# Performance work log

Hardware: AMD Instinct MI355X
Metric: run time of the kernel (lower is better)

## Reference

```python
import jax, jax.numpy as jnp
import numpy as np

R = 16            # DFL bins (reg_max)
C = 80            # num classes
STRIDES = (8, 16, 32)
CONF = 0.25
IOU_T = 0.45
MAX_DET = 300
K_PRE = 1024      # fixed pre-NMS candidate count (static-shape stand-in for torch's boolean mask)
CLS_OFFSET = 4096.0  # > max image coord; class-aware NMS offset (torchvision batched_nms trick)


def setup_inputs() -> dict:
    key = jax.random.key(0)
    k0, k1, k2 = jax.random.split(key, 3)
    B, CH = 16, 4 * R + C
    return {
        "p0": jax.random.normal(k0, (B, CH, 80, 80), jnp.float32),
        "p1": jax.random.normal(k1, (B, CH, 40, 40), jnp.float32),
        "p2": jax.random.normal(k2, (B, CH, 20, 20), jnp.float32),
        "h_img": 640,
        "w_img": 640,
    }


def _decode_level(p, stride):
    # p: (B, 4R+C, H, W)
    B, _, H, W = p.shape
    box_logits = p[:, : 4 * R].reshape(B, 4, R, H * W)
    bins = jnp.arange(R, dtype=p.dtype)
    # DFLIntegral: softmax over bins, expectation -> l,t,r,b distances (in stride units)
    ltrb = jnp.einsum('bkrm,r->bkm', jax.nn.softmax(box_logits, axis=2), bins) * stride  # (B,4,HW)
    yv, xv = jnp.meshgrid(jnp.arange(H, dtype=p.dtype), jnp.arange(W, dtype=p.dtype), indexing='ij')
    cx = (xv.reshape(-1) + 0.5) * stride  # (HW,)
    cy = (yv.reshape(-1) + 0.5) * stride
    x1 = cx[None] - ltrb[:, 0]
    y1 = cy[None] - ltrb[:, 1]
    x2 = cx[None] + ltrb[:, 2]
    y2 = cy[None] + ltrb[:, 3]
    boxes = jnp.stack((x1, y1, x2, y2), axis=2)  # (B, HW, 4)
    scores = jax.nn.sigmoid(p[:, 4 * R:].reshape(B, C, H * W))  # (B, C, HW)
    smax = scores.max(axis=1)      # (B, HW)
    labels = scores.argmax(axis=1)  # (B, HW) int
    return boxes, smax, labels


def _pairwise_iou(b):
    # b: (K, 4) xyxy
    area = (b[:, 2] - b[:, 0]) * (b[:, 3] - b[:, 1])
    lt = jnp.maximum(b[:, None, :2], b[None, :, :2])
    rb = jnp.minimum(b[:, None, 2:], b[None, :, 2:])
    wh = jnp.clip(rb - lt, 0.0)
    inter = wh[..., 0] * wh[..., 1]
    return inter / (area[:, None] + area[None, :] - inter + 1e-7)


def _nms_single(boxes, smax, labels):
    # boxes (A,4), smax (A,), labels (A,)
    s = jnp.where(smax > CONF, smax, -1.0)
    sv, idx = jax.lax.top_k(s, K_PRE)          # score-sorted pre-NMS candidates
    bsel = boxes[idx]                           # (K,4)
    lsel = labels[idx]
    vsel = sv > CONF                            # candidate passes conf filter
    boff = bsel + lsel[:, None].astype(bsel.dtype) * CLS_OFFSET  # class-aware offset
    iou = _pairwise_iou(boff)
    iou = iou * (1.0 - jnp.eye(K_PRE, dtype=iou.dtype))  # no self-suppression

    def step(supp, i):
        keep_i = jnp.logical_and(~supp[i], vsel[i])
        supp = jnp.where(keep_i, supp | (iou[i] > IOU_T), supp)
        return supp, keep_i

    _, keep = jax.lax.scan(step, jnp.zeros(K_PRE, bool), jnp.arange(K_PRE))
    rank = jnp.cumsum(keep) - 1
    slot = jnp.where(keep & (rank < MAX_DET), rank, MAX_DET)  # dump overflow into dummy slot
    boxes_out = jnp.zeros((MAX_DET + 1, 4), bsel.dtype).at[slot].set(bsel)[:MAX_DET]
    scores_out = jnp.zeros((MAX_DET + 1,), sv.dtype).at[slot].set(sv)[:MAX_DET]
    labels_out = jnp.full((MAX_DET + 1,), -1, jnp.int32).at[slot].set(lsel.astype(jnp.int32))[:MAX_DET]
    n = jnp.minimum(keep.sum(), MAX_DET)
    valid_out = jnp.arange(MAX_DET) < n
    return boxes_out, scores_out, labels_out, valid_out


def reference(p0, p1, p2, h_img, w_img):
    parts = [_decode_level(p, s) for p, s in zip((p0, p1, p2), STRIDES)]
    boxes = jnp.concatenate([x[0] for x in parts], axis=1)   # (B, A, 4)
    smax = jnp.concatenate([x[1] for x in parts], axis=1)    # (B, A)
    labels = jnp.concatenate([x[2] for x in parts], axis=1)  # (B, A)
    hi = jnp.array([w_img - 1, h_img - 1, w_img - 1, h_img - 1], boxes.dtype)
    boxes = jnp.clip(boxes, 0.0, hi)
    return jax.vmap(_nms_single)(boxes, smax, labels)
```

## Files before the change

kernel.cpp:

```cpp
#include <hip/hip_runtime.h>
#include <stdint.h>

#define NR 16
#define NC 80
#define NA 8400
#define NB 16
#define KPRE 1024
#define MAXDET 300
#define CONF_T 0.25f
#define IOU_THR 0.45f

__device__ __forceinline__ float read_dim(const void* p) {
  int iv = *(const int*)p;
  return (iv > 0 && iv < (1 << 20)) ? (float)iv : *(const float*)p;
}

__device__ __forceinline__ const float* level_ptr(const float* p0, const float* p1,
                                                  const float* p2, int a, int& HW,
                                                  int& W, float& stride, int& m) {
  if (a < 6400)      { HW = 6400; W = 80; stride = 8.f;  m = a;        return p0; }
  else if (a < 8000) { HW = 1600; W = 40; stride = 16.f; m = a - 6400; return p1; }
  else               { HW = 400;  W = 20; stride = 32.f; m = a - 8000; return p2; }
}

__device__ __forceinline__ uint64_t readlane64(uint64_t v, int lane) {
  uint32_t lo = (uint32_t)__builtin_amdgcn_readlane((int)(uint32_t)v, lane);
  uint32_t hi = (uint32_t)__builtin_amdgcn_readlane((int)(uint32_t)(v >> 32), lane);
  return ((uint64_t)hi << 32) | lo;
}

__global__ __launch_bounds__(256) void k_decode(
    const float* __restrict__ p0, const float* __restrict__ p1,
    const float* __restrict__ p2, const void* __restrict__ hp,
    const void* __restrict__ wp, float4* __restrict__ boxes,
    uint32_t* __restrict__ keys, int* __restrict__ labels) {
  int gid = blockIdx.x * 256 + threadIdx.x;
  int aid = gid >> 2, k = gid & 3;
  int b = aid / NA, a = aid - b * NA;
  int HW, W, m; float stride;
  const float* p = level_ptr(p0, p1, p2, a, HW, W, stride, m);
  const float* base = p + (size_t)b * (4 * NR + NC) * HW + m;

  float v[NR]; float mx = -3.4e38f;
#pragma unroll
  for (int r = 0; r < NR; ++r) { v[r] = base[(size_t)(k * NR + r) * HW]; mx = fmaxf(mx, v[r]); }
  float se = 0.f, sn = 0.f;
#pragma unroll
  for (int r = 0; r < NR; ++r) { float e = expf(v[r] - mx); se += e; sn += e * (float)r; }
  float dk = sn / se * stride;

  float ml = -3.4e38f; int mc = NC;
#pragma unroll 4
  for (int c = 0; c < 20; ++c) {
    int ch = 4 * c + k;
    float vv = base[(size_t)(4 * NR + ch) * HW];
    if (vv > ml) { ml = vv; mc = ch; }
  }
#pragma unroll
  for (int off = 1; off < 4; off <<= 1) {
    float ov = __shfl_xor(ml, off);
    int oc = __shfl_xor(mc, off);
    if (ov > ml || (ov == ml && oc < mc)) { ml = ov; mc = oc; }
  }
  int lane = threadIdx.x & 63;
  int bl = lane & ~3;
  float dl = __shfl(dk, bl), dt = __shfl(dk, bl + 1);
  float dr = __shfl(dk, bl + 2), db = __shfl(dk, bl + 3);

  if (k == 0) {
    int x = m % W, y = m / W;
    float cx = ((float)x + 0.5f) * stride, cy = ((float)y + 0.5f) * stride;
    float hx = read_dim(wp) - 1.f, hy = read_dim(hp) - 1.f;
    boxes[aid] = make_float4(fminf(fmaxf(cx - dl, 0.f), hx),
                             fminf(fmaxf(cy - dt, 0.f), hy),
                             fminf(fmaxf(cx + dr, 0.f), hx),
                             fminf(fmaxf(cy + db, 0.f), hy));
  } else if (k == 1) {
    float smax = 1.f / (1.f + expf(-ml));
    float s = smax > CONF_T ? smax : -1.0f;
    uint32_t bt = __float_as_uint(s);
    keys[aid] = (bt & 0x80000000u) ? ~bt : (bt | 0x80000000u);
  } else if (k == 2) {
    labels[aid] = mc;
  }
}

__global__ __launch_bounds__(1024) void k_selcomp(const uint32_t* __restrict__ keys,
                                                  uint64_t* __restrict__ cmp,
                                                  int* __restrict__ ccount) {
  __shared__ uint32_t skeys[NA];
  __shared__ uint32_t whist[16][256];
  __shared__ uint32_t hsum[256], ssuf[256];
  __shared__ int s_b1, s_rem, s_t16, s_cnt;
  int img = blockIdx.x, tid = threadIdx.x;
  int w = tid >> 6, lane = tid & 63;
  const uint32_t* kb = keys + (size_t)img * NA;
  for (int j = tid; j < NA; j += 1024) skeys[j] = kb[j];
  if (tid == 0) s_cnt = 0;

  for (int j = tid; j < 16 * 256; j += 1024) ((uint32_t*)whist)[j] = 0;
  __syncthreads();
  for (int j = tid; j < NA; j += 1024) atomicAdd(&whist[w][skeys[j] >> 24], 1u);
  __syncthreads();
  if (tid < 256) { uint32_t s = 0; for (int i = 0; i < 16; ++i) s += whist[i][tid]; hsum[tid] = s; }
  __syncthreads();
  if (tid < 256) { uint32_t s = 0; for (int j = tid; j < 256; ++j) s += hsum[j]; ssuf[tid] = s; }
  __syncthreads();
  if (tid < 256) {
    uint32_t ab = (tid == 255) ? 0u : ssuf[tid + 1];
    if (ssuf[tid] >= KPRE && ab < KPRE) { s_b1 = tid; s_rem = KPRE - (int)ab; }
  }
  __syncthreads();
  int b1 = s_b1, rem = s_rem;
  __syncthreads();

  for (int j = tid; j < 16 * 256; j += 1024) ((uint32_t*)whist)[j] = 0;
  __syncthreads();
  for (int j = tid; j < NA; j += 1024) {
    uint32_t k = skeys[j];
    if ((int)(k >> 24) == b1) atomicAdd(&whist[w][(k >> 16) & 0xFF], 1u);
  }
  __syncthreads();
  if (tid < 256) { uint32_t s = 0; for (int i = 0; i < 16; ++i) s += whist[i][tid]; hsum[tid] = s; }
  __syncthreads();
  if (tid < 256) { uint32_t s = 0; for (int j = tid; j < 256; ++j) s += hsum[j]; ssuf[tid] = s; }
  __syncthreads();
  if (tid < 256) {
    int ab = (tid == 255) ? 0 : (int)ssuf[tid + 1];
    if ((int)ssuf[tid] >= rem && ab < rem) s_t16 = (b1 << 8) | tid;
  }
  __syncthreads();
  uint32_t t16 = (uint32_t)s_t16;

  for (int j0 = 0; j0 < NA; j0 += 1024) {
    int j = j0 + tid;
    uint32_t k = (j < NA) ? skeys[j] : 0;
    bool pass = (j < NA) && ((k >> 16) >= t16);
    uint64_t mask = __ballot(pass);
    int pre = __popcll(mask & ((1ull << lane) - 1ull));
    int wc = __popcll(mask);
    int base = 0;
    if (lane == 0) base = wc ? atomicAdd(&s_cnt, wc) : 0;
    base = __shfl(base, 0);
    if (pass)
      cmp[(size_t)img * NA + base + pre] =
          ((uint64_t)k << 32) | (uint64_t)(0xFFFFFFFFu - (uint32_t)j);
  }
  __syncthreads();
  if (tid == 0) ccount[img] = s_cnt;
}

__global__ __launch_bounds__(256) void k_rank2(
    const uint64_t* __restrict__ cmp, const int* __restrict__ ccount,
    const float4* __restrict__ boxes, const int* __restrict__ labels,
    float4* __restrict__ selbox, float4* __restrict__ selboff,
    float* __restrict__ selscore, int* __restrict__ sellab) {
  __shared__ uint64_t sk[2048];
  int img = blockIdx.y;
  int M = ccount[img]; if (M > NA) M = NA;
  if (blockIdx.x * 256 >= M) return;
  int c = blockIdx.x * 256 + threadIdx.x;
  uint64_t kc = (c < M) ? cmp[(size_t)img * NA + c] : 0;
  int rank = 0;
  for (int j0 = 0; j0 < M; j0 += 2048) {
    int nchunk = min(2048, M - j0);
    __syncthreads();
    for (int j = threadIdx.x; j < nchunk; j += 256)
      sk[j] = cmp[(size_t)img * NA + j0 + j];
    __syncthreads();
    if (c < M) {
      int j = 0;
      for (; j + 4 <= nchunk; j += 4) {
        rank += (int)(sk[j] > kc) + (int)(sk[j + 1] > kc) +
                (int)(sk[j + 2] > kc) + (int)(sk[j + 3] > kc);
      }
      for (; j < nchunk; ++j) rank += (int)(sk[j] > kc);
    }
  }
  if (c < M && rank < KPRE) {
    int a = (int)(0xFFFFFFFFu - (uint32_t)kc);
    uint32_t uk = (uint32_t)(kc >> 32);
    uint32_t bits = (uk & 0x80000000u) ? (uk & 0x7FFFFFFFu) : ~uk;
    float s = __uint_as_float(bits);
    int lab = labels[img * NA + a];
    float4 bx = boxes[img * NA + a];
    float off = (float)lab * 4096.0f;
    int o = img * KPRE + rank;
    selbox[o] = bx;
    selboff[o] = make_float4(bx.x + off, bx.y + off, bx.z + off, bx.w + off);
    selscore[o] = s;
    sellab[o] = lab;
  }
}

__global__ __launch_bounds__(256) void k_iou(const float4* __restrict__ selboff,
                                             uint64_t* __restrict__ rowmask) {
  __shared__ float4 bb[KPRE];
  int img = blockIdx.y;
  for (int j = threadIdx.x; j < KPRE; j += 256) bb[j] = selboff[img * KPRE + j];
  __syncthreads();
  int i = blockIdx.x * 16 + (threadIdx.x & 15);
  int w = threadIdx.x >> 4;
  float4 bi = bb[i];
  float ai = (bi.z - bi.x) * (bi.w - bi.y);
  uint64_t bits = 0;
  for (int jj = 0; jj < 64; ++jj) {
    int j = w * 64 + jj;
    float4 bj = bb[j];
    float lx = fmaxf(bi.x, bj.x), ly = fmaxf(bi.y, bj.y);
    float rx = fminf(bi.z, bj.z), ry = fminf(bi.w, bj.w);
    float iw = fmaxf(rx - lx, 0.f), ih = fmaxf(ry - ly, 0.f);
    float inter = iw * ih;
    float aj = (bj.z - bj.x) * (bj.w - bj.y);
    float iou = inter / (ai + aj - inter + 1e-7f);
    bits |= (uint64_t)((iou > IOU_THR) && (j != i)) << jj;
  }
  rowmask[(size_t)img * 16384 + (size_t)w * 1024 + i] = bits;
}

__global__ __launch_bounds__(64) void k_scan(
    const uint64_t* __restrict__ rowmask, const float4* __restrict__ selbox,
    const float* __restrict__ selscore, const int* __restrict__ sellab,
    float* __restrict__ out) {
  __shared__ float lsc[KPRE];
  __shared__ uint64_t buf[2][16 * 65];
  __shared__ int keepidx[MAXDET];
  int img = blockIdx.x, lane = threadIdx.x;
  const uint64_t* g = rowmask + (size_t)img * 16384;

  for (int j = lane; j < KPRE; j += 64) lsc[j] = selscore[img * KPRE + j];

  {
    uint64_t r0[16];
#pragma unroll
    for (int t = 0; t < 16; ++t) r0[t] = g[t * 1024 + lane];
#pragma unroll
    for (int t = 0; t < 16; ++t) buf[0][t * 65 + lane] = r0[t];
  }
  asm volatile("" ::: "memory");

  uint64_t remv = 0;
  int n = 0;
  for (int c = 0; c < 16; ++c) {
    uint64_t rn[16];
    if (c + 1 < 16) {
#pragma unroll
      for (int t = 0; t < 16; ++t) rn[t] = g[t * 1024 + (c + 1) * 64 + lane];
    }
    const uint64_t* B = buf[c & 1];
    uint64_t m = B[c * 65 + lane];
    float sc = lsc[c * 64 + lane];
    uint64_t vmask = __ballot(sc > CONF_T);
    uint64_t cur = readlane64(remv, c);
    uint64_t kmask = 0;
#pragma unroll
    for (int ii = 0; ii < 64; ++ii) {
      if (((vmask >> ii) & 1ull) && !((cur >> ii) & 1ull)) {
        cur |= readlane64(m, ii);
        kmask |= (1ull << ii);
        if (lane == 0 && n < MAXDET) keepidx[n] = c * 64 + ii;
        n++;
      }
    }
    if (lane < 16) {
      uint64_t km = kmask;
      while (km) {
        int ii2 = __ffsll((unsigned long long)km) - 1;
        km &= km - 1;
        remv |= B[lane * 65 + ii2];
      }
    }
    if (!((vmask >> 63) & 1ull) || n >= MAXDET) break;
    if (c + 1 < 16) {
#pragma unroll
      for (int t = 0; t < 16; ++t) buf[(c + 1) & 1][t * 65 + lane] = rn[t];
    }
    asm volatile("" ::: "memory");
  }

  asm volatile("" ::: "memory");
  float* ob = out;
  float* os = out + NB * MAXDET * 4;
  float* ol = out + NB * MAXDET * 5;
  float* ov = out + NB * MAXDET * 6;
  int nk = n < MAXDET ? n : MAXDET;
  for (int s0 = 0; s0 < MAXDET; s0 += 64) {
    int slot = s0 + lane;
    if (slot >= MAXDET) break;
    bool v = slot < nk;
    float4 bx = make_float4(0.f, 0.f, 0.f, 0.f);
    float scv = 0.f, lbv = -1.f;
    if (v) {
      int i = keepidx[slot];
      bx = selbox[img * KPRE + i];
      scv = lsc[i];
      lbv = (float)sellab[img * KPRE + i];
    }
    ((float4*)ob)[img * MAXDET + slot] = bx;
    os[img * MAXDET + slot] = scv;
    ol[img * MAXDET + slot] = lbv;
    ov[img * MAXDET + slot] = v ? 1.0f : 0.0f;
  }
}

extern "C" void kernel_launch(void* const* d_in, const int* in_sizes, int n_in,
                              void* d_out, int out_size, void* d_ws, size_t ws_size,
                              hipStream_t stream) {
  const float* p0 = (const float*)d_in[0];
  const float* p1 = (const float*)d_in[1];
  const float* p2 = (const float*)d_in[2];
  const void* hp = d_in[3];
  const void* wp = d_in[4];

  char* ws = (char*)d_ws;
  float4*   boxes    = (float4*)(ws + 0);
  uint64_t* rowmask  = (uint64_t*)(ws + 0);
  uint32_t* keys     = (uint32_t*)(ws + 2150400);
  int*      labels   = (int*)(ws + 2688000);
  float4*   selbox   = (float4*)(ws + 3225600);
  float4*   selboff  = (float4*)(ws + 3487744);
  float*    selscore = (float*)(ws + 3749888);
  int*      sellab   = (int*)(ws + 3815424);
  int*      ccount   = (int*)(ws + 3880960);
  uint64_t* cmp      = (uint64_t*)(ws + 3881024);

  k_decode<<<(NB * NA * 4) / 256, 256, 0, stream>>>(p0, p1, p2, hp, wp,
                                                    boxes, keys, labels);
  k_selcomp<<<NB, 1024, 0, stream>>>(keys, cmp, ccount);
  dim3 rg((NA + 255) / 256, NB);
  k_rank2<<<rg, 256, 0, stream>>>(cmp, ccount, boxes, labels,
                                  selbox, selboff, selscore, sellab);
  dim3 ig(KPRE / 16, NB);
  k_iou<<<ig, 256, 0, stream>>>(selboff, rowmask);
  k_scan<<<NB, 64, 0, stream>>>(rowmask, selbox, selscore, sellab,
                                (float*)d_out);
}
```

Measured before the change: 207.1 us.

## Fuse the decode/select/rank/IoU/scan pipeline into one cooperative kernel

```diff
diff --git a/kernel.cpp b/kernel.cpp
--- a/kernel.cpp
+++ b/kernel.cpp
@@ -1,5 +1,8 @@
 #include <hip/hip_runtime.h>
+#include <hip/hip_cooperative_groups.h>
 #include <stdint.h>
+
+namespace cg = cooperative_groups;
 
 #define NR 16
 #define NC 80
@@ -9,6 +12,9 @@
 #define MAXDET 300
 #define CONF_T 0.25f
 #define IOU_THR 0.45f
+#define GRIDN 256
+#define GRIDT (GRIDN * 256)
+#define APAD 8448
 
 __device__ __forceinline__ float read_dim(const void* p) {
   int iv = *(const int*)p;
@@ -29,277 +35,298 @@
   return ((uint64_t)hi << 32) | lo;
 }
 
-__global__ __launch_bounds__(256) void k_decode(
+union Smem {
+  struct {
+    uint32_t skeys[NA];
+    uint32_t whist[4][257];
+    uint32_t hsum[256], ssuf[256];
+  } sel;
+  struct { uint64_t sk[2048]; } rank;
+  struct { float4 bb[KPRE]; } iou;
+  struct {
+    float lsc[KPRE];
+    uint64_t buf[2][16 * 65];
+    int keepidx[MAXDET];
+  } scan;
+};
+
+__global__ __launch_bounds__(256) void k_mega(
     const float* __restrict__ p0, const float* __restrict__ p1,
     const float* __restrict__ p2, const void* __restrict__ hp,
     const void* __restrict__ wp, float4* __restrict__ boxes,
-    uint32_t* __restrict__ keys, int* __restrict__ labels) {
-  int gid = blockIdx.x * 256 + threadIdx.x;
-  int aid = gid >> 2, k = gid & 3;
-  int b = aid / NA, a = aid - b * NA;
-  int HW, W, m; float stride;
-  const float* p = level_ptr(p0, p1, p2, a, HW, W, stride, m);
-  const float* base = p + (size_t)b * (4 * NR + NC) * HW + m;
-
-  float v[NR]; float mx = -3.4e38f;
-#pragma unroll
-  for (int r = 0; r < NR; ++r) { v[r] = base[(size_t)(k * NR + r) * HW]; mx = fmaxf(mx, v[r]); }
-  float se = 0.f, sn = 0.f;
-#pragma unroll
-  for (int r = 0; r < NR; ++r) { float e = expf(v[r] - mx); se += e; sn += e * (float)r; }
-  float dk = sn / se * stride;
-
-  float ml = -3.4e38f; int mc = NC;
+    uint32_t* __restrict__ keys, int* __restrict__ labels,
+    uint64_t* __restrict__ cmp, int* __restrict__ ccount,
+    int* __restrict__ tstar, float4* __restrict__ selbox,
+    float4* __restrict__ selboff, float* __restrict__ selscore,
+    int* __restrict__ sellab, uint64_t* __restrict__ rowmask,
+    float* __restrict__ out) {
+  cg::grid_group grid = cg::this_grid();
+  __shared__ Smem sm;
+  __shared__ int s_b1, s_rem, s_t16;
+  int tid = threadIdx.x;
+  int lane = tid & 63;
+  int gtid = blockIdx.x * 256 + tid;
+
+  {
+    float hx = read_dim(wp) - 1.f, hy = read_dim(hp) - 1.f;
+    for (int wk = gtid; wk < NB * NA * 4; wk += GRIDT) {
+      int aid = wk >> 2, k = wk & 3;
+      int b = aid / NA, a = aid - b * NA;
+      int HW, W, m; float stride;
+      const float* p = level_ptr(p0, p1, p2, a, HW, W, stride, m);
+      const float* base = p + (size_t)b * (4 * NR + NC) * HW + m;
+
+      float v[NR]; float mx = -3.4e38f;
+#pragma unroll
+      for (int r = 0; r < NR; ++r) { v[r] = base[(size_t)(k * NR + r) * HW]; mx = fmaxf(mx, v[r]); }
+      float se = 0.f, sn = 0.f;
+#pragma unroll
+      for (int r = 0; r < NR; ++r) { float e = expf(v[r] - mx); se += e; sn += e * (float)r; }
+      float dk = sn / se * stride;
+
+      float ml = -3.4e38f; int mc = NC;
 #pragma unroll 4
-  for (int c = 0; c < 20; ++c) {
-    int ch = 4 * c + k;
-    float vv = base[(size_t)(4 * NR + ch) * HW];
-    if (vv > ml) { ml = vv; mc = ch; }
-  }
-#pragma unroll
-  for (int off = 1; off < 4; off <<= 1) {
-    float ov = __shfl_xor(ml, off);
-    int oc = __shfl_xor(mc, off);
-    if (ov > ml || (ov == ml && oc < mc)) { ml = ov; mc = oc; }
-  }
-  int lane = threadIdx.x & 63;
-  int bl = lane & ~3;
-  float dl = __shfl(dk, bl), dt = __shfl(dk, bl + 1);
-  float dr = __shfl(dk, bl + 2), db = __shfl(dk, bl + 3);
-
-  if (k == 0) {
-    int x = m % W, y = m / W;
-    float cx = ((float)x + 0.5f) * stride, cy = ((float)y + 0.5f) * stride;
-    float hx = read_dim(wp) - 1.f, hy = read_dim(hp) - 1.f;
-    boxes[aid] = make_float4(fminf(fmaxf(cx - dl, 0.f), hx),
-                             fminf(fmaxf(cy - dt, 0.f), hy),
-                             fminf(fmaxf(cx + dr, 0.f), hx),
-                             fminf(fmaxf(cy + db, 0.f), hy));
-  } else if (k == 1) {
-    float smax = 1.f / (1.f + expf(-ml));
-    float s = smax > CONF_T ? smax : -1.0f;
-    uint32_t bt = __float_as_uint(s);
-    keys[aid] = (bt & 0x80000000u) ? ~bt : (bt | 0x80000000u);
-  } else if (k == 2) {
-    labels[aid] = mc;
-  }
-}
-
-__global__ __launch_bounds__(1024) void k_selcomp(const uint32_t* __restrict__ keys,
-                                                  uint64_t* __restrict__ cmp,
-                                                  int* __restrict__ ccount) {
-  __shared__ uint32_t skeys[NA];
-  __shared__ uint32_t whist[16][256];
-  __shared__ uint32_t hsum[256], ssuf[256];
-  __shared__ int s_b1, s_rem, s_t16, s_cnt;
-  int img = blockIdx.x, tid = threadIdx.x;
-  int w = tid >> 6, lane = tid & 63;
-  const uint32_t* kb = keys + (size_t)img * NA;
-  for (int j = tid; j < NA; j += 1024) skeys[j] = kb[j];
-  if (tid == 0) s_cnt = 0;
-
-  for (int j = tid; j < 16 * 256; j += 1024) ((uint32_t*)whist)[j] = 0;
-  __syncthreads();
-  for (int j = tid; j < NA; j += 1024) atomicAdd(&whist[w][skeys[j] >> 24], 1u);
-  __syncthreads();
-  if (tid < 256) { uint32_t s = 0; for (int i = 0; i < 16; ++i) s += whist[i][tid]; hsum[tid] = s; }
-  __syncthreads();
-  if (tid < 256) { uint32_t s = 0; for (int j = tid; j < 256; ++j) s += hsum[j]; ssuf[tid] = s; }
-  __syncthreads();
-  if (tid < 256) {
-    uint32_t ab = (tid == 255) ? 0u : ssuf[tid + 1];
-    if (ssuf[tid] >= KPRE && ab < KPRE) { s_b1 = tid; s_rem = KPRE - (int)ab; }
-  }
-  __syncthreads();
-  int b1 = s_b1, rem = s_rem;
-  __syncthreads();
-
-  for (int j = tid; j < 16 * 256; j += 1024) ((uint32_t*)whist)[j] = 0;
-  __syncthreads();
-  for (int j = tid; j < NA; j += 1024) {
-    uint32_t k = skeys[j];
-    if ((int)(k >> 24) == b1) atomicAdd(&whist[w][(k >> 16) & 0xFF], 1u);
-  }
-  __syncthreads();
-  if (tid < 256) { uint32_t s = 0; for (int i = 0; i < 16; ++i) s += whist[i][tid]; hsum[tid] = s; }
-  __syncthreads();
-  if (tid < 256) { uint32_t s = 0; for (int j = tid; j < 256; ++j) s += hsum[j]; ssuf[tid] = s; }
-  __syncthreads();
-  if (tid < 256) {
-    int ab = (tid == 255) ? 0 : (int)ssuf[tid + 1];
-    if ((int)ssuf[tid] >= rem && ab < rem) s_t16 = (b1 << 8) | tid;
-  }
-  __syncthreads();
-  uint32_t t16 = (uint32_t)s_t16;
-
-  for (int j0 = 0; j0 < NA; j0 += 1024) {
-    int j = j0 + tid;
-    uint32_t k = (j < NA) ? skeys[j] : 0;
-    bool pass = (j < NA) && ((k >> 16) >= t16);
+      for (int c = 0; c < 20; ++c) {
+        int ch = 4 * c + k;
+        float vv = base[(size_t)(4 * NR + ch) * HW];
+        if (vv > ml) { ml = vv; mc = ch; }
+      }
+#pragma unroll
+      for (int off = 1; off < 4; off <<= 1) {
+        float ov = __shfl_xor(ml, off);
+        int oc = __shfl_xor(mc, off);
+        if (ov > ml || (ov == ml && oc < mc)) { ml = ov; mc = oc; }
+      }
+      int bl = lane & ~3;
+      float dl = __shfl(dk, bl), dt = __shfl(dk, bl + 1);
+      float dr = __shfl(dk, bl + 2), db = __shfl(dk, bl + 3);
+
+      if (k == 0) {
+        int x = m % W, y = m / W;
+        float cx = ((float)x + 0.5f) * stride, cy = ((float)y + 0.5f) * stride;
+        boxes[aid] = make_float4(fminf(fmaxf(cx - dl, 0.f), hx),
+                                 fminf(fmaxf(cy - dt, 0.f), hy),
+                                 fminf(fmaxf(cx + dr, 0.f), hx),
+                                 fminf(fmaxf(cy + db, 0.f), hy));
+      } else if (k == 1) {
+        float smax = 1.f / (1.f + expf(-ml));
+        float s = smax > CONF_T ? smax : -1.0f;
+        uint32_t bt = __float_as_uint(s);
+        keys[aid] = (bt & 0x80000000u) ? ~bt : (bt | 0x80000000u);
+      } else if (k == 2) {
+        labels[aid] = mc;
+      }
+    }
+  }
+  grid.sync();
+
+  if (blockIdx.x < NB) {
+    int img = blockIdx.x;
+    int w4 = tid >> 6;
+    const uint32_t* kb = keys + (size_t)img * NA;
+    for (int j = tid; j < NA; j += 256) sm.sel.skeys[j] = kb[j];
+    if (tid == 0) ccount[img] = 0;
+
+    for (int j = tid; j < 4 * 257; j += 256) ((uint32_t*)sm.sel.whist)[j] = 0;
+    __syncthreads();
+    for (int j = tid; j < NA; j += 256) atomicAdd(&sm.sel.whist[w4][sm.sel.skeys[j] >> 24], 1u);
+    __syncthreads();
+    { uint32_t s = 0; for (int i = 0; i < 4; ++i) s += sm.sel.whist[i][tid]; sm.sel.hsum[tid] = s; }
+    __syncthreads();
+    { uint32_t s = 0; for (int j = tid; j < 256; ++j) s += sm.sel.hsum[j]; sm.sel.ssuf[tid] = s; }
+    __syncthreads();
+    {
+      uint32_t ab = (tid == 255) ? 0u : sm.sel.ssuf[tid + 1];
+      if (sm.sel.ssuf[tid] >= KPRE && ab < KPRE) { s_b1 = tid; s_rem = KPRE - (int)ab; }
+    }
+    __syncthreads();
+    int b1 = s_b1, rem = s_rem;
+    __syncthreads();
+
+    for (int j = tid; j < 4 * 257; j += 256) ((uint32_t*)sm.sel.whist)[j] = 0;
+    __syncthreads();
+    for (int j = tid; j < NA; j += 256) {
+      uint32_t k = sm.sel.skeys[j];
+      if ((int)(k >> 24) == b1) atomicAdd(&sm.sel.whist[w4][(k >> 16) & 0xFF], 1u);
+    }
+    __syncthreads();
+    { uint32_t s = 0; for (int i = 0; i < 4; ++i) s += sm.sel.whist[i][tid]; sm.sel.hsum[tid] = s; }
+    __syncthreads();
+    { uint32_t s = 0; for (int j = tid; j < 256; ++j) s += sm.sel.hsum[j]; sm.sel.ssuf[tid] = s; }
+    __syncthreads();
+    {
+      int ab = (tid == 255) ? 0 : (int)sm.sel.ssuf[tid + 1];
+      if ((int)sm.sel.ssuf[tid] >= rem && ab < rem) s_t16 = (b1 << 8) | tid;
+    }
+    __syncthreads();
+    if (tid == 0) tstar[img] = s_t16;
+  }
+  grid.sync();
+
+  for (int wk = gtid; wk < NB * APAD; wk += GRIDT) {
+    int img = wk / APAD;
+    int a = wk - img * APAD;
+    uint32_t k = 0; bool pass = false;
+    if (a < NA) {
+      k = keys[(size_t)img * NA + a];
+      pass = (int)(k >> 16) >= tstar[img];
+    }
     uint64_t mask = __ballot(pass);
     int pre = __popcll(mask & ((1ull << lane) - 1ull));
     int wc = __popcll(mask);
     int base = 0;
-    if (lane == 0) base = wc ? atomicAdd(&s_cnt, wc) : 0;
+    if (lane == 0 && wc) base = atomicAdd(&ccount[img], wc);
     base = __shfl(base, 0);
     if (pass)
       cmp[(size_t)img * NA + base + pre] =
-          ((uint64_t)k << 32) | (uint64_t)(0xFFFFFFFFu - (uint32_t)j);
-  }
-  __syncthreads();
-  if (tid == 0) ccount[img] = s_cnt;
-}
-
-__global__ __launch_bounds__(256) void k_rank2(
-    const uint64_t* __restrict__ cmp, const int* __restrict__ ccount,
-    const float4* __restrict__ boxes, const int* __restrict__ labels,
-    float4* __restrict__ selbox, float4* __restrict__ selboff,
-    float* __restrict__ selscore, int* __restrict__ sellab) {
-  __shared__ uint64_t sk[2048];
-  int img = blockIdx.y;
-  int M = ccount[img]; if (M > NA) M = NA;
-  if (blockIdx.x * 256 >= M) return;
-  int c = blockIdx.x * 256 + threadIdx.x;
-  uint64_t kc = (c < M) ? cmp[(size_t)img * NA + c] : 0;
-  int rank = 0;
-  for (int j0 = 0; j0 < M; j0 += 2048) {
-    int nchunk = min(2048, M - j0);
-    __syncthreads();
-    for (int j = threadIdx.x; j < nchunk; j += 256)
-      sk[j] = cmp[(size_t)img * NA + j0 + j];
-    __syncthreads();
-    if (c < M) {
-      int j = 0;
-      for (; j + 4 <= nchunk; j += 4) {
-        rank += (int)(sk[j] > kc) + (int)(sk[j + 1] > kc) +
-                (int)(sk[j + 2] > kc) + (int)(sk[j + 3] > kc);
-      }
-      for (; j < nchunk; ++j) rank += (int)(sk[j] > kc);
-    }
-  }
-  if (c < M && rank < KPRE) {
-    int a = (int)(0xFFFFFFFFu - (uint32_t)kc);
-    uint32_t uk = (uint32_t)(kc >> 32);
-    uint32_t bits = (uk & 0x80000000u) ? (uk & 0x7FFFFFFFu) : ~uk;
-    float s = __uint_as_float(bits);
-    int lab = labels[img * NA + a];
-    float4 bx = boxes[img * NA + a];
-    float off = (float)lab * 4096.0f;
-    int o = img * KPRE + rank;
-    selbox[o] = bx;
-    selboff[o] = make_float4(bx.x + off, bx.y + off, bx.z + off, bx.w + off);
-    selscore[o] = s;
-    sellab[o] = lab;
-  }
-}
-
-__global__ __launch_bounds__(256) void k_iou(const float4* __restrict__ selboff,
-                                             uint64_t* __restrict__ rowmask) {
-  __shared__ float4 bb[KPRE];
-  int img = blockIdx.y;
-  for (int j = threadIdx.x; j < KPRE; j += 256) bb[j] = selboff[img * KPRE + j];
-  __syncthreads();
-  int i = blockIdx.x * 16 + (threadIdx.x & 15);
-  int w = threadIdx.x >> 4;
-  float4 bi = bb[i];
-  float ai = (bi.z - bi.x) * (bi.w - bi.y);
-  uint64_t bits = 0;
-  for (int jj = 0; jj < 64; ++jj) {
-    int j = w * 64 + jj;
-    float4 bj = bb[j];
-    float lx = fmaxf(bi.x, bj.x), ly = fmaxf(bi.y, bj.y);
-    float rx = fminf(bi.z, bj.z), ry = fminf(bi.w, bj.w);
-    float iw = fmaxf(rx - lx, 0.f), ih = fmaxf(ry - ly, 0.f);
-    float inter = iw * ih;
-    float aj = (bj.z - bj.x) * (bj.w - bj.y);
-    float iou = inter / (ai + aj - inter + 1e-7f);
-    bits |= (uint64_t)((iou > IOU_THR) && (j != i)) << jj;
-  }
-  rowmask[(size_t)img * 16384 + (size_t)w * 1024 + i] = bits;
-}
-
-__global__ __launch_bounds__(64) void k_scan(
-    const uint64_t* __restrict__ rowmask, const float4* __restrict__ selbox,
-    const float* __restrict__ selscore, const int* __restrict__ sellab,
-    float* __restrict__ out) {
-  __shared__ float lsc[KPRE];
-  __shared__ uint64_t buf[2][16 * 65];
-  __shared__ int keepidx[MAXDET];
-  int img = blockIdx.x, lane = threadIdx.x;
-  const uint64_t* g = rowmask + (size_t)img * 16384;
-
-  for (int j = lane; j < KPRE; j += 64) lsc[j] = selscore[img * KPRE + j];
+          ((uint64_t)k << 32) | (uint64_t)(0xFFFFFFFFu - (uint32_t)a);
+  }
+  grid.sync();
+
+  for (int u = blockIdx.x; u < NB * 33; u += GRIDN) {
+    int img = u / 33, blk = u - img * 33;
+    int M = ccount[img]; if (M > NA) M = NA;
+    if (blk * 256 >= M) continue;
+    int c = blk * 256 + tid;
+    uint64_t kc = (c < M) ? cmp[(size_t)img * NA + c] : 0;
+    int rank = 0;
+    for (int j0 = 0; j0 < M; j0 += 2048) {
+      int nchunk = min(2048, M - j0);
+      __syncthreads();
+      for (int j = tid; j < nchunk; j += 256)
+        sm.rank.sk[j] = cmp[(size_t)img * NA + j0 + j];
+      __syncthreads();
+      if (c < M) {
+        int j = 0;
+        for (; j + 4 <= nchunk; j += 4) {
+          rank += (int)(sm.rank.sk[j] > kc) + (int)(sm.rank.sk[j + 1] > kc) +
+                  (int)(sm.rank.sk[j + 2] > kc) + (int)(sm.rank.sk[j + 3] > kc);
+        }
+        for (; j < nchunk; ++j) rank += (int)(sm.rank.sk[j] > kc);
+      }
+    }
+    __syncthreads();
+    if (c < M && rank < KPRE) {
+      int a = (int)(0xFFFFFFFFu - (uint32_t)kc);
+      uint32_t uk = (uint32_t)(kc >> 32);
+      uint32_t bits = (uk & 0x80000000u) ? (uk & 0x7FFFFFFFu) : ~uk;
+      float s = __uint_as_float(bits);
+      int lab = labels[img * NA + a];
+      float4 bx = boxes[img * NA + a];
+      float off = (float)lab * 4096.0f;
+      int o = img * KPRE + rank;
+      selbox[o] = bx;
+      selboff[o] = make_float4(bx.x + off, bx.y + off, bx.z + off, bx.w + off);
+      selscore[o] = s;
+      sellab[o] = lab;
+    }
+  }
+  grid.sync();
 
   {
-    uint64_t r0[16];
-#pragma unroll
-    for (int t = 0; t < 16; ++t) r0[t] = g[t * 1024 + lane];
-#pragma unroll
-    for (int t = 0; t < 16; ++t) buf[0][t * 65 + lane] = r0[t];
-  }
-  asm volatile("" ::: "memory");
-
-  uint64_t remv = 0;
-  int n = 0;
-  for (int c = 0; c < 16; ++c) {
-    uint64_t rn[16];
-    if (c + 1 < 16) {
-#pragma unroll
-      for (int t = 0; t < 16; ++t) rn[t] = g[t * 1024 + (c + 1) * 64 + lane];
-    }
-    const uint64_t* B = buf[c & 1];
-    uint64_t m = B[c * 65 + lane];
-    float sc = lsc[c * 64 + lane];
-    uint64_t vmask = __ballot(sc > CONF_T);
-    uint64_t cur = readlane64(remv, c);
-    uint64_t kmask = 0;
-#pragma unroll
-    for (int ii = 0; ii < 64; ++ii) {
-      if (((vmask >> ii) & 1ull) && !((cur >> ii) & 1ull)) {
-        cur |= readlane64(m, ii);
-        kmask |= (1ull << ii);
-        if (lane == 0 && n < MAXDET) keepidx[n] = c * 64 + ii;
-        n++;
-      }
-    }
-    if (lane < 16) {
-      uint64_t km = kmask;
-      while (km) {
-        int ii2 = __ffsll((unsigned long long)km) - 1;
-        km &= km - 1;
-        remv |= B[lane * 65 + ii2];
-      }
-    }
-    if (!((vmask >> 63) & 1ull) || n >= MAXDET) break;
-    if (c + 1 < 16) {
-#pragma unroll
-      for (int t = 0; t < 16; ++t) buf[(c + 1) & 1][t * 65 + lane] = rn[t];
+    int img = blockIdx.x >> 4, seg = blockIdx.x & 15;
+    for (int j = tid; j < KPRE; j += 256) sm.iou.bb[j] = selboff[img * KPRE + j];
+    __syncthreads();
+#pragma unroll
+    for (int t = 0; t < 4; ++t) {
+      int pid = tid + t * 256;
+      int row = seg * 64 + (pid >> 4);
+      int w = pid & 15;
+      float4 bi = sm.iou.bb[row];
+      float ai = (bi.z - bi.x) * (bi.w - bi.y);
+      uint64_t bits = 0;
+      for (int jj = 0; jj < 64; ++jj) {
+        int j = w * 64 + jj;
+        float4 bj = sm.iou.bb[j];
+        float lx = fmaxf(bi.x, bj.x), ly = fmaxf(bi.y, bj.y);
+        float rx = fminf(bi.z, bj.z), ry = fminf(bi.w, bj.w);
+        float iw = fmaxf(rx - lx, 0.f), ih = fmaxf(ry - ly, 0.f);
+        float inter = iw * ih;
+        float aj = (bj.z - bj.x) * (bj.w - bj.y);
+        float iou = inter / (ai + aj - inter + 1e-7f);
+        bits |= (uint64_t)((iou > IOU_THR) && (j != row)) << jj;
+      }
+      rowmask[(size_t)img * 16384 + (size_t)w * 1024 + row] = bits;
+    }
+  }
+  grid.sync();
+
+  if (blockIdx.x < NB && tid < 64) {
+    int img = blockIdx.x;
+    const uint64_t* g = rowmask + (size_t)img * 16384;
+    for (int j = lane; j < KPRE; j += 64) sm.scan.lsc[j] = selscore[img * KPRE + j];
+
+    {
+      uint64_t r0[16];
+#pragma unroll
+      for (int t = 0; t < 16; ++t) r0[t] = g[t * 1024 + lane];
+#pragma unroll
+      for (int t = 0; t < 16; ++t) sm.scan.buf[0][t * 65 + lane] = r0[t];
     }
     asm volatile("" ::: "memory");
-  }
-
-  asm volatile("" ::: "memory");
-  float* ob = out;
-  float* os = out + NB * MAXDET * 4;
-  float* ol = out + NB * MAXDET * 5;
-  float* ov = out + NB * MAXDET * 6;
-  int nk = n < MAXDET ? n : MAXDET;
-  for (int s0 = 0; s0 < MAXDET; s0 += 64) {
-    int slot = s0 + lane;
-    if (slot >= MAXDET) break;
-    bool v = slot < nk;
-    float4 bx = make_float4(0.f, 0.f, 0.f, 0.f);
-    float scv = 0.f, lbv = -1.f;
-    if (v) {
-      int i = keepidx[slot];
-      bx = selbox[img * KPRE + i];
-      scv = lsc[i];
-      lbv = (float)sellab[img * KPRE + i];
-    }
-    ((float4*)ob)[img * MAXDET + slot] = bx;
-    os[img * MAXDET + slot] = scv;
-    ol[img * MAXDET + slot] = lbv;
-    ov[img * MAXDET + slot] = v ? 1.0f : 0.0f;
+
+    uint64_t remv = 0;
+    int n = 0;
+    for (int c = 0; c < 16; ++c) {
+      uint64_t rn[16];
+      if (c + 1 < 16) {
+#pragma unroll
+        for (int t = 0; t < 16; ++t) rn[t] = g[t * 1024 + (c + 1) * 64 + lane];
+      }
+      const uint64_t* B = sm.scan.buf[c & 1];
+      uint64_t m = B[c * 65 + lane];
+      float sc = sm.scan.lsc[c * 64 + lane];
+      uint64_t vmask = __ballot(sc > CONF_T);
+      uint64_t cur = readlane64(remv, c);
+      uint64_t kmask = 0;
+#pragma unroll
+      for (int ii = 0; ii < 64; ++ii) {
+        if (((vmask >> ii) & 1ull) && !((cur >> ii) & 1ull)) {
+          cur |= readlane64(m, ii);
+          kmask |= (1ull << ii);
+          if (lane == 0 && n < MAXDET) sm.scan.keepidx[n] = c * 64 + ii;
+          n++;
+        }
+      }
+      if (lane < 16) {
+        uint64_t km = kmask;
+        while (km) {
+          int ii2 = __ffsll((unsigned long long)km) - 1;
+          km &= km - 1;
+          remv |= B[lane * 65 + ii2];
+        }
+      }
+      if (!((vmask >> 63) & 1ull) || n >= MAXDET) break;
+      if (c + 1 < 16) {
+#pragma unroll
+        for (int t = 0; t < 16; ++t) sm.scan.buf[(c + 1) & 1][t * 65 + lane] = rn[t];
+      }
+      asm volatile("" ::: "memory");
+    }
+
+    asm volatile("" ::: "memory");
+    float* ob = out;
+    float* os = out + NB * MAXDET * 4;
+    float* ol = out + NB * MAXDET * 5;
+    float* ov = out + NB * MAXDET * 6;
+    int nk = n < MAXDET ? n : MAXDET;
+    for (int s0 = 0; s0 < MAXDET; s0 += 64) {
+      int slot = s0 + lane;
+      if (slot >= MAXDET) break;
+      bool v = slot < nk;
+      float4 bx = make_float4(0.f, 0.f, 0.f, 0.f);
+      float scv = 0.f, lbv = -1.f;
+      if (v) {
+        int i = sm.scan.keepidx[slot];
+        bx = selbox[img * KPRE + i];
+        scv = sm.scan.lsc[i];
+        lbv = (float)sellab[img * KPRE + i];
+      }
+      ((float4*)ob)[img * MAXDET + slot] = bx;
+      os[img * MAXDET + slot] = scv;
+      ol[img * MAXDET + slot] = lbv;
+      ov[img * MAXDET + slot] = v ? 1.0f : 0.0f;
+    }
   }
 }
 
@@ -322,16 +349,13 @@
   float*    selscore = (float*)(ws + 3749888);
   int*      sellab   = (int*)(ws + 3815424);
   int*      ccount   = (int*)(ws + 3880960);
-  uint64_t* cmp      = (uint64_t*)(ws + 3881024);
-
-  k_decode<<<(NB * NA * 4) / 256, 256, 0, stream>>>(p0, p1, p2, hp, wp,
-                                                    boxes, keys, labels);
-  k_selcomp<<<NB, 1024, 0, stream>>>(keys, cmp, ccount);
-  dim3 rg((NA + 255) / 256, NB);
-  k_rank2<<<rg, 256, 0, stream>>>(cmp, ccount, boxes, labels,
-                                  selbox, selboff, selscore, sellab);
-  dim3 ig(KPRE / 16, NB);
-  k_iou<<<ig, 256, 0, stream>>>(selboff, rowmask);
-  k_scan<<<NB, 64, 0, stream>>>(rowmask, selbox, selscore, sellab,
-                                (float*)d_out);
-}
+  int*      tstar    = (int*)(ws + 3881024);
+  uint64_t* cmp      = (uint64_t*)(ws + 3881088);
+  float*    outp     = (float*)d_out;
+
+  void* kargs[] = {&p0, &p1, &p2, &hp, &wp, &boxes, &keys, &labels,
+                   &cmp, &ccount, &tstar, &selbox, &selboff, &selscore,
+                   &sellab, &rowmask, &outp};
+  hipLaunchCooperativeKernel(reinterpret_cast<void*>(k_mega), dim3(GRIDN),
+                             dim3(256), kargs, 0, stream);
+}
```

Result: slower. 416.7 us (+101.2%).
